# Kernel optimization log

Measured on AMD Instinct MI355X. Metric: run time of the kernel, lower is better.

Reference implementation:

```python
import jax, jax.numpy as jnp
import numpy as np

HIDDEN = 2048
N_HEADS = 32
N_KV_HEADS = 4
HEAD_DIM = 128
EPS = 1e-6
ROPE_THETA = 1000000.0
B, S = 1, 2048


def setup_inputs() -> dict:
    key = jax.random.key(0)
    ks = jax.random.split(key, 7)
    scale = 0.02
    return {
        "hidden_states": jax.random.normal(ks[0], (B, S, HIDDEN), jnp.float32),
        "wq": jax.random.normal(ks[1], (HIDDEN, N_HEADS * HEAD_DIM), jnp.float32) * scale,
        "wk": jax.random.normal(ks[2], (HIDDEN, N_KV_HEADS * HEAD_DIM), jnp.float32) * scale,
        "wv": jax.random.normal(ks[3], (HIDDEN, N_KV_HEADS * HEAD_DIM), jnp.float32) * scale,
        "wo": jax.random.normal(ks[4], (N_HEADS * HEAD_DIM, HIDDEN), jnp.float32) * scale,
        "q_norm_w": jnp.ones((HEAD_DIM,), jnp.float32),
        "k_norm_w": jnp.ones((HEAD_DIM,), jnp.float32),
    }


def _rmsnorm(x, w, eps=EPS):
    # RMSNorm over last (head_dim) axis, as in Qwen3MoeRMSNorm applied per-head
    var = jnp.mean(jnp.square(x), axis=-1, keepdims=True)
    return x * jax.lax.rsqrt(var + eps) * w


def _rope_cos_sin(seq_len, dtype):
    inv_freq = 1.0 / (ROPE_THETA ** (jnp.arange(0, HEAD_DIM, 2, dtype=jnp.float32) / HEAD_DIM))
    pos = jnp.arange(seq_len, dtype=jnp.float32)
    freqs = pos[:, None] * inv_freq[None, :]          # [S, dh/2]
    emb = jnp.concatenate([freqs, freqs], axis=-1)    # [S, dh]
    return jnp.cos(emb).astype(dtype), jnp.sin(emb).astype(dtype)


def _rotate_half(x):
    h = x.shape[-1] // 2
    return jnp.concatenate([-x[..., h:], x[..., :h]], axis=-1)


def reference(hidden_states, wq, wk, wv, wo, q_norm_w, k_norm_w):
    b, s, _ = hidden_states.shape
    # QKV projections (bias-free)
    q = (hidden_states @ wq).reshape(b, s, N_HEADS, HEAD_DIM)
    k = (hidden_states @ wk).reshape(b, s, N_KV_HEADS, HEAD_DIM)
    v = (hidden_states @ wv).reshape(b, s, N_KV_HEADS, HEAD_DIM)
    # per-head RMSNorm on Q and K
    q = _rmsnorm(q, q_norm_w)
    k = _rmsnorm(k, k_norm_w)
    # RoPE (prefill, start_pos = 0)
    cos, sin = _rope_cos_sin(s, q.dtype)              # [S, dh]
    cos = cos[None, :, None, :]
    sin = sin[None, :, None, :]
    q = q * cos + _rotate_half(q) * sin
    k = k * cos + _rotate_half(k) * sin
    # GQA: repeat KV heads to match Q heads
    groups = N_HEADS // N_KV_HEADS
    k = jnp.repeat(k, groups, axis=2)                 # [B,S,nH,dh]
    v = jnp.repeat(v, groups, axis=2)
    # causal SDPA
    scaling = HEAD_DIM ** -0.5
    scores = jnp.einsum("bqhd,bkhd->bhqk", q, k) * scaling
    causal = jnp.tril(jnp.ones((s, s), dtype=bool))
    scores = jnp.where(causal[None, None], scores, jnp.finfo(scores.dtype).min)
    probs = jax.nn.softmax(scores, axis=-1)
    attn = jnp.einsum("bhqk,bkhd->bqhd", probs, v)    # [B,S,nH,dh]
    attn = attn.reshape(b, s, N_HEADS * HEAD_DIM)
    return attn @ wo
```

## Files before the change

kernel.cpp:

```cpp
#include <hip/hip_runtime.h>
#include <stdint.h>

typedef unsigned short u16;
typedef __bf16 bf16x8 __attribute__((ext_vector_type(8)));
typedef float f32x4 __attribute__((ext_vector_type(4)));

#define SEQ 2048
#define QKV_N 5120
#define QN 4096

#if __has_builtin(__builtin_amdgcn_exp2f)
#define EXP2F __builtin_amdgcn_exp2f
#else
#define EXP2F exp2f
#endif

#define QSC (0.08838834764831845f * 1.4426950408889634f)
#define MLOG2E 17.312340490667560f

#define WAIT_VM(n) asm volatile("s_waitcnt vmcnt(" #n ")" ::: "memory")
#define WAIT_LGKM asm volatile("s_waitcnt lgkmcnt(0)" ::: "memory")
#define FENCE asm volatile("" ::: "memory")
#define BARRIER_RAW do { FENCE; __builtin_amdgcn_s_barrier(); FENCE; } while (0)

__device__ __forceinline__ u16 f2bf(float f) {
  union { float f; unsigned u; } v; v.f = f;
  unsigned r = v.u + 0x7fffu + ((v.u >> 16) & 1u);
  return (u16)(r >> 16);
}
__device__ __forceinline__ u16 f2bf_fast(float f) {
  union { float f; unsigned u; } v; v.f = f;
  return (u16)((v.u + 0x8000u) >> 16);
}
__device__ __forceinline__ float bf2f(u16 b) {
  union { unsigned u; float f; } v; v.u = ((unsigned)b) << 16;
  return v.f;
}

__device__ __forceinline__ void gl2lds16(const void* g, void* l) {
  __builtin_amdgcn_global_load_lds((const __attribute__((address_space(1))) void*)g,
                                   (__attribute__((address_space(3))) void*)l, 16, 0, 0);
}

__global__ __launch_bounds__(256) void k_prep(const float* __restrict__ hidden,
                                              const float* __restrict__ wq, const float* __restrict__ wk,
                                              const float* __restrict__ wv, const float* __restrict__ wo,
                                              u16* __restrict__ hid_bf, u16* __restrict__ WT,
                                              u16* __restrict__ woT) {
  __shared__ float t[32][33];
  int bx = blockIdx.x;
  if (bx < 4096) {
    int i = (bx * 256 + threadIdx.x) * 4;
    float4 v = *(const float4*)(hidden + i);
    ushort4 o;
    o.x = f2bf(v.x); o.y = f2bf(v.y); o.z = f2bf(v.z); o.w = f2bf(v.w);
    *(ushort4*)(hid_bf + i) = o;
    return;
  }
  const float* src; u16* dst; int R, C, cx, cy;
  if (bx < 4096 + 8192) {
    int local = bx - 4096; src = wq; dst = WT; R = 2048; C = 4096;
    cx = local & 127; cy = local >> 7;
  } else if (bx < 4096 + 8192 + 1024) {
    int local = bx - (4096 + 8192); src = wk; dst = WT + (size_t)4096 * 2048; R = 2048; C = 512;
    cx = local & 15; cy = local >> 4;
  } else if (bx < 4096 + 8192 + 2048) {
    int local = bx - (4096 + 8192 + 1024); src = wv; dst = WT + (size_t)4608 * 2048; R = 2048; C = 512;
    cx = local & 15; cy = local >> 4;
  } else {
    int local = bx - (4096 + 8192 + 2048); src = wo; dst = woT; R = 4096; C = 2048;
    cx = local & 63; cy = local >> 6;
  }
  int c0 = cx * 32, r0 = cy * 32;
  int j = threadIdx.x & 31, i0 = threadIdx.x >> 5;
#pragma unroll
  for (int p = 0; p < 4; ++p) {
    int r = i0 + p * 8;
    t[r][j] = src[(size_t)(r0 + r) * C + c0 + j];
  }
  __syncthreads();
#pragma unroll
  for (int p = 0; p < 4; ++p) {
    int r = i0 + p * 8;
    dst[(size_t)(c0 + r) * R + r0 + j] = f2bf(t[j][r]);
  }
}

__global__ __launch_bounds__(256) void k_gemm160(const u16* __restrict__ A, const u16* __restrict__ BT,
                                                 u16* __restrict__ C, int M, int N, int K) {
  __shared__ u16 As[2][128 * 64];
  __shared__ u16 Bs[2][160 * 64];
  const int tid = threadIdx.x;
  const int w = tid >> 6, lane = tid & 63, quad = lane >> 4, l15 = lane & 15;
  const int m0 = blockIdx.y * 128, n0 = blockIdx.x * 160;
  const int mw = (w & 1) * 64, nw = (w >> 1) * 80;

  f32x4 acc[4][5];
#pragma unroll
  for (int i = 0; i < 4; ++i)
#pragma unroll
    for (int j = 0; j < 5; ++j) acc[i][j] = {0.f, 0.f, 0.f, 0.f};

  auto stage = [&](int kt, int buf) {
    const int k0 = kt << 6;
#pragma unroll
    for (int p = 0; p < 4; ++p) {
      int ci = (w * 4 + p) * 64 + lane;
      int row = ci >> 3, gc = (ci & 7) ^ (row & 7);
      gl2lds16(A + (size_t)(m0 + row) * K + k0 + gc * 8, &As[buf][(w * 4 + p) * 512]);
    }
#pragma unroll
    for (int p = 0; p < 5; ++p) {
      int ci = (w * 5 + p) * 64 + lane;
      int row = ci >> 3, gc = (ci & 7) ^ (row & 7);
      gl2lds16(BT + (size_t)(n0 + row) * K + k0 + gc * 8, &Bs[buf][(w * 5 + p) * 512]);
    }
  };

  const int nk = K >> 6;
  stage(0, 0);
  for (int kt = 0; kt < nk; ++kt) {
    WAIT_LGKM;
    BARRIER_RAW;
    if (kt + 1 < nk) {
      stage(kt + 1, (kt + 1) & 1);
      WAIT_VM(9);
    } else {
      WAIT_VM(0);
    }
    BARRIER_RAW;
    const u16* Ac = As[kt & 1];
    const u16* Bc = Bs[kt & 1];
#pragma unroll
    for (int kk = 0; kk < 2; ++kk) {
      bf16x8 a[4], b[5];
#pragma unroll
      for (int mt = 0; mt < 4; ++mt) {
        int row = mw + mt * 16 + l15;
        a[mt] = *(const bf16x8*)(Ac + row * 64 + (((kk * 4 + quad) ^ (row & 7)) * 8));
      }
#pragma unroll
      for (int nt = 0; nt < 5; ++nt) {
        int row = nw + nt * 16 + l15;
        b[nt] = *(const bf16x8*)(Bc + row * 64 + (((kk * 4 + quad) ^ (row & 7)) * 8));
      }
#pragma unroll
      for (int mt = 0; mt < 4; ++mt)
#pragma unroll
        for (int nt = 0; nt < 5; ++nt)
          acc[mt][nt] = __builtin_amdgcn_mfma_f32_16x16x32_bf16(a[mt], b[nt], acc[mt][nt], 0, 0, 0);
    }
  }
#pragma unroll
  for (int mt = 0; mt < 4; ++mt)
#pragma unroll
    for (int nt = 0; nt < 5; ++nt)
#pragma unroll
      for (int r = 0; r < 4; ++r) {
        int row = m0 + mw + mt * 16 + quad * 4 + r;
        int col = n0 + nw + nt * 16 + l15;
        C[(size_t)row * N + col] = f2bf(acc[mt][nt][r]);
      }
}

__global__ __launch_bounds__(256) void k_gemm_sk(const u16* __restrict__ A, const u16* __restrict__ BT,
                                                 float* __restrict__ C, int M, int N, int K) {
  __shared__ u16 As[2][128 * 64];
  __shared__ u16 Bs[2][128 * 64];
  const int tid = threadIdx.x;
  const int w = tid >> 6, lane = tid & 63, quad = lane >> 4, l15 = lane & 15;
  const int m0 = blockIdx.y * 128, n0 = blockIdx.x * 128;
  const int mw = (w & 1) * 64, nw = (w >> 1) * 64;
  const int khalf = K >> 1;
  const int kbase = blockIdx.z * khalf;

  f32x4 acc[4][4];
#pragma unroll
  for (int i = 0; i < 4; ++i)
#pragma unroll
    for (int j = 0; j < 4; ++j) acc[i][j] = {0.f, 0.f, 0.f, 0.f};

  auto stage = [&](int kt, int buf) {
    const int k0 = kbase + (kt << 6);
#pragma unroll
    for (int p = 0; p < 4; ++p) {
      int ci = (w * 4 + p) * 64 + lane;
      int row = ci >> 3, gc = (ci & 7) ^ (row & 7);
      gl2lds16(A + (size_t)(m0 + row) * K + k0 + gc * 8, &As[buf][(w * 4 + p) * 512]);
      gl2lds16(BT + (size_t)(n0 + row) * K + k0 + gc * 8, &Bs[buf][(w * 4 + p) * 512]);
    }
  };

  const int nk = khalf >> 6;
  stage(0, 0);
  for (int kt = 0; kt < nk; ++kt) {
    WAIT_LGKM;
    BARRIER_RAW;
    if (kt + 1 < nk) {
      stage(kt + 1, (kt + 1) & 1);
      WAIT_VM(8);
    } else {
      WAIT_VM(0);
    }
    BARRIER_RAW;
    const u16* Ac = As[kt & 1];
    const u16* Bc = Bs[kt & 1];
#pragma unroll
    for (int kk = 0; kk < 2; ++kk) {
      bf16x8 a[4], b[4];
#pragma unroll
      for (int mt = 0; mt < 4; ++mt) {
        int row = mw + mt * 16 + l15;
        a[mt] = *(const bf16x8*)(Ac + row * 64 + (((kk * 4 + quad) ^ (row & 7)) * 8));
      }
#pragma unroll
      for (int nt = 0; nt < 4; ++nt) {
        int row = nw + nt * 16 + l15;
        b[nt] = *(const bf16x8*)(Bc + row * 64 + (((kk * 4 + quad) ^ (row & 7)) * 8));
      }
#pragma unroll
      for (int mt = 0; mt < 4; ++mt)
#pragma unroll
        for (int nt = 0; nt < 4; ++nt)
          acc[mt][nt] = __builtin_amdgcn_mfma_f32_16x16x32_bf16(a[mt], b[nt], acc[mt][nt], 0, 0, 0);
    }
  }
#pragma unroll
  for (int mt = 0; mt < 4; ++mt)
#pragma unroll
    for (int nt = 0; nt < 4; ++nt)
#pragma unroll
      for (int r = 0; r < 4; ++r) {
        int row = m0 + mw + mt * 16 + quad * 4 + r;
        int col = n0 + nw + nt * 16 + l15;
        atomicAdd(&C[(size_t)row * N + col], acc[mt][nt][r]);
      }
}

__global__ __launch_bounds__(256) void k_post(const u16* __restrict__ QKV,
                                              const float* __restrict__ qw, const float* __restrict__ kw,
                                              u16* __restrict__ qb, u16* __restrict__ kb,
                                              u16* __restrict__ vt) {
  __shared__ u16 t[32][34];
  int bx = blockIdx.x;
  if (bx < 2048) {
    int s = bx;
    int w = threadIdx.x >> 6, lane = threadIdx.x & 63;
    const u16* row = QKV + (size_t)s * QKV_N;
    float inv_freq = EXP2F(-(float)lane * (19.931568569324174f / 64.0f));
    float fr = (float)s * inv_freq;
    float sn, cs;
    __sincosf(fr, &sn, &cs);
    float qw0 = qw[lane], qw1 = qw[lane + 64];
    float kw0 = kw[lane], kw1 = kw[lane + 64];
    for (int item = w; item < 36; item += 4) {
      bool isq = item < 32;
      int h = isq ? item : item - 32;
      int base = isq ? h * 128 : 4096 + h * 128;
      float x0 = bf2f(row[base + lane]), x1 = bf2f(row[base + 64 + lane]);
      float ss = x0 * x0 + x1 * x1;
#pragma unroll
      for (int off = 1; off < 64; off <<= 1) ss += __shfl_xor(ss, off);
      float rr = rsqrtf(ss * (1.0f / 128.0f) + 1e-6f);
      float n0 = x0 * rr * (isq ? qw0 : kw0), n1 = x1 * rr * (isq ? qw1 : kw1);
      float y0 = n0 * cs - n1 * sn;
      float y1 = n1 * cs + n0 * sn;
      if (isq) {
        size_t o = (size_t)s * QN + h * 128 + lane;
        qb[o] = f2bf(y0 * QSC);
        qb[o + 64] = f2bf(y1 * QSC);
      } else {
        size_t o = ((size_t)h * SEQ + s) * 128 + lane;
        kb[o] = f2bf(y0);
        kb[o + 64] = f2bf(y1);
      }
    }
    return;
  }
  int local = bx - 2048;
  int s0 = (local & 63) * 32, d0 = ((local >> 6) & 3) * 32, h = local >> 8;
  int j = threadIdx.x & 31, i0 = threadIdx.x >> 5;
#pragma unroll
  for (int p = 0; p < 4; ++p) {
    int r = i0 + p * 8;
    t[r][j] = QKV[(size_t)(s0 + r) * QKV_N + 4608 + h * 128 + d0 + j];
  }
  __syncthreads();
#pragma unroll
  for (int p = 0; p < 4; ++p) {
    int r = i0 + p * 8;
    vt[((size_t)h * 128 + d0 + r) * SEQ + s0 + j] = t[j][r];
  }
}

__global__ __launch_bounds__(256, 2) void k_flash(const u16* __restrict__ qb_, const u16* __restrict__ kb,
                                                  const u16* __restrict__ vt, u16* __restrict__ attn) {
  __shared__ u16 Ks[2][64 * 128];
  __shared__ u16 Vts[2][128 * 64];
  __shared__ u16 Ps[4][2048];
  const int bx = blockIdx.x;
  const int head = bx & 31;
  const int a = bx >> 5;
  const int kvh = head >> 3;
  const int tid = threadIdx.x, w = tid >> 6, lane = tid & 63, quad = lane >> 4, l15 = lane & 15;
  const int rA = a * 64 + w * 16;
  const int rB = (31 - a) * 64 + w * 16;

  bf16x8 qf[2][4];
#pragma unroll
  for (int mt = 0; mt < 2; ++mt) {
    const int rbase = mt ? rB : rA;
    const u16* qrow = qb_ + (size_t)(rbase + l15) * QN + head * 128;
#pragma unroll
    for (int ks = 0; ks < 4; ++ks) qf[mt][ks] = *(const bf16x8*)(qrow + ks * 32 + quad * 8);
  }
  f32x4 o[2][8];
#pragma unroll
  for (int mt = 0; mt < 2; ++mt)
#pragma unroll
    for (int i = 0; i < 8; ++i) o[mt][i] = {0.f, 0.f, 0.f, 0.f};
  float lr[2][4] = {{0.f, 0.f, 0.f, 0.f}, {0.f, 0.f, 0.f, 0.f}};

  const u16* kbase = kb + (size_t)kvh * SEQ * 128;
  const u16* vbase = vt + (size_t)kvh * 128 * SEQ;
  u16* pw = Ps[w];

  auto stage = [&](int ti, int buf) {
    const int t0 = ti * 64;
#pragma unroll
    for (int p = 0; p < 4; ++p) {
      int ci = (w * 4 + p) * 64 + lane;
      {
        int row = ci >> 4, gc = (ci & 15) ^ (row & 15);
        gl2lds16(kbase + (size_t)(t0 + row) * 128 + gc * 8, &Ks[buf][(w * 4 + p) * 512]);
      }
      {
        int d = ci >> 3, gc = (ci & 7) ^ (d & 7);
        gl2lds16(vbase + (size_t)d * SEQ + t0 + gc * 8, &Vts[buf][(w * 4 + p) * 512]);
      }
    }
  };

  const int nT = 32 - a;
  stage(0, 0);
  for (int ti = 0; ti < nT; ++ti) {
    const int t0 = ti * 64;
    WAIT_LGKM;
    BARRIER_RAW;
    if (ti + 1 < nT) {
      stage(ti + 1, (ti + 1) & 1);
      WAIT_VM(8);
    } else {
      WAIT_VM(0);
    }
    BARRIER_RAW;
    const u16* Kc = Ks[ti & 1];
    const u16* Vc = Vts[ti & 1];

    const bool aA = t0 < rA + 16;
    {
      f32x4 sa[2][4];
#pragma unroll
      for (int mt = 0; mt < 2; ++mt)
#pragma unroll
        for (int nt = 0; nt < 4; ++nt) sa[mt][nt] = {0.f, 0.f, 0.f, 0.f};
#pragma unroll
      for (int nt = 0; nt < 4; ++nt) {
        int row = nt * 16 + l15;
#pragma unroll
        for (int ks = 0; ks < 4; ++ks) {
          bf16x8 kf = *(const bf16x8*)(Kc + row * 128 + (((ks * 4 + quad) ^ (row & 15)) * 8));
          if (aA) sa[0][nt] = __builtin_amdgcn_mfma_f32_16x16x32_bf16(qf[0][ks], kf, sa[0][nt], 0, 0, 0);
          sa[1][nt] = __builtin_amdgcn_mfma_f32_16x16x32_bf16(qf[1][ks], kf, sa[1][nt], 0, 0, 0);
        }
      }
#pragma unroll
      for (int mt = 0; mt < 2; ++mt) {
        if (mt == 0 && !aA) continue;
        const int rl = mt ? rB : rA;
        const bool domask = (t0 + 63 > rl);
        u16* pm = pw + mt * 1024;
#pragma unroll
        for (int nt = 0; nt < 4; ++nt)
#pragma unroll
          for (int r = 0; r < 4; ++r) {
            float p = EXP2F(sa[mt][nt][r] - MLOG2E);
            if (domask) {
              int tcol = t0 + nt * 16 + l15;
              int qrow = rl + quad * 4 + r;
              p = (tcol > qrow) ? 0.f : p;
            }
            sa[mt][nt][r] = p;
            pm[(quad * 4 + r) * 64 + ((nt ^ quad) << 4) + l15] = f2bf_fast(p);
          }
#pragma unroll
        for (int r = 0; r < 4; ++r)
          lr[mt][r] += sa[mt][0][r] + sa[mt][1][r] + sa[mt][2][r] + sa[mt][3][r];
      }
      WAIT_LGKM;
#pragma unroll
      for (int ks2 = 0; ks2 < 2; ++ks2) {
        int col = (ks2 * 32 + quad * 8) ^ ((l15 >> 2) << 4);
        bf16x8 pa0, pa1;
        if (aA) pa0 = *(const bf16x8*)(pw + l15 * 64 + col);
        pa1 = *(const bf16x8*)(pw + 1024 + l15 * 64 + col);
#pragma unroll
        for (int nt2 = 0; nt2 < 8; ++nt2) {
          int d = nt2 * 16 + l15;
          bf16x8 vf = *(const bf16x8*)(Vc + d * 64 + (((ks2 * 4 + quad) ^ (d & 7)) * 8));
          if (aA) o[0][nt2] = __builtin_amdgcn_mfma_f32_16x16x32_bf16(pa0, vf, o[0][nt2], 0, 0, 0);
          o[1][nt2] = __builtin_amdgcn_mfma_f32_16x16x32_bf16(pa1, vf, o[1][nt2], 0, 0, 0);
        }
      }
    }
  }
#pragma unroll
  for (int mt = 0; mt < 2; ++mt) {
    const int rbase = mt ? rB : rA;
    float inv[4];
#pragma unroll
    for (int r = 0; r < 4; ++r) {
      float s = lr[mt][r];
      s += __shfl_xor(s, 1);
      s += __shfl_xor(s, 2);
      s += __shfl_xor(s, 4);
      s += __shfl_xor(s, 8);
      inv[r] = 1.0f / s;
    }
#pragma unroll
    for (int nt2 = 0; nt2 < 8; ++nt2)
#pragma unroll
      for (int r = 0; r < 4; ++r) {
        size_t idx = (size_t)(rbase + quad * 4 + r) * QN + head * 128 + nt2 * 16 + l15;
        attn[idx] = f2bf_fast(o[mt][nt2][r] * inv[r]);
      }
  }
}

extern "C" void kernel_launch(void* const* d_in, const int* in_sizes, int n_in,
                              void* d_out, int out_size, void* d_ws, size_t ws_size,
                              hipStream_t stream) {
  const float* hidden = (const float*)d_in[0];
  const float* wq = (const float*)d_in[1];
  const float* wk = (const float*)d_in[2];
  const float* wv = (const float*)d_in[3];
  const float* wo = (const float*)d_in[4];
  const float* qnw = (const float*)d_in[5];
  const float* knw = (const float*)d_in[6];
  float* out = (float*)d_out;

  char* ws = (char*)d_ws;
  u16* hid_bf = (u16*)(ws);
  u16* WT = (u16*)(ws + 8388608);
  u16* woT = (u16*)(ws + 29360128);
  u16* QKV = (u16*)(ws + 46137344);
  u16* q_bf = (u16*)(ws + 88080384);
  u16* k_bf = (u16*)(ws + 104857600);
  u16* vt = (u16*)(ws + 106954752);
  u16* attn = (u16*)(ws + 109051904);

  hipMemsetAsync(d_out, 0, (size_t)2048 * 2048 * 4, stream);
  k_prep<<<22528, 256, 0, stream>>>(hidden, wq, wk, wv, wo, hid_bf, WT, woT);
  k_gemm160<<<dim3(32, 16), 256, 0, stream>>>(hid_bf, WT, QKV, 2048, 5120, 2048);
  k_post<<<3072, 256, 0, stream>>>(QKV, qnw, knw, q_bf, k_bf, vt);
  k_flash<<<512, 256, 0, stream>>>(q_bf, k_bf, vt, attn);
  k_gemm_sk<<<dim3(16, 16, 2), 256, 0, stream>>>(attn, woT, out, 2048, 2048, 4096);
}
```

Baseline: 323.8 us.

## Restructure flash attention to 128-row Q tiles with 8 waves and 128-key tiles

The flash kernel moves from 4-wave blocks that each handle a paired light and heavy 64-row Q tile to 8-wave blocks that each handle one 128-row Q tile. Blocks are ordered heaviest first, and K/V tiles grow to 128 keys. K stays double-buffered, while V becomes single-buffered and is loaded during the QK^T and softmax phase. s_setprio is raised around the MFMA loops. This is meant to double K/V reuse in LDS per block and cut per-tile overhead, at the cost of losing the causal pairing balance and of more LDS per block (about 104KB), which limits occupancy.

Measured after the change: 304.2 us. 6.0% less time.

```diff
diff --git a/kernel.cpp b/kernel.cpp
--- a/kernel.cpp
+++ b/kernel.cpp
@@ -293,148 +293,136 @@
   }
 }
 
-__global__ __launch_bounds__(256, 2) void k_flash(const u16* __restrict__ qb_, const u16* __restrict__ kb,
-                                                  const u16* __restrict__ vt, u16* __restrict__ attn) {
-  __shared__ u16 Ks[2][64 * 128];
-  __shared__ u16 Vts[2][128 * 64];
-  __shared__ u16 Ps[4][2048];
+__global__ __launch_bounds__(512) void k_flash(const u16* __restrict__ qb_, const u16* __restrict__ kb,
+                                               const u16* __restrict__ vt, u16* __restrict__ attn) {
+  __shared__ u16 Ks[2][128 * 128];
+  __shared__ u16 Vts[128 * 128];
+  __shared__ u16 Ps[8][16 * 128];
   const int bx = blockIdx.x;
   const int head = bx & 31;
-  const int a = bx >> 5;
+  const int qblk = 15 - (bx >> 5);
   const int kvh = head >> 3;
+  const int q0 = qblk * 128;
   const int tid = threadIdx.x, w = tid >> 6, lane = tid & 63, quad = lane >> 4, l15 = lane & 15;
-  const int rA = a * 64 + w * 16;
-  const int rB = (31 - a) * 64 + w * 16;
-
-  bf16x8 qf[2][4];
-#pragma unroll
-  for (int mt = 0; mt < 2; ++mt) {
-    const int rbase = mt ? rB : rA;
-    const u16* qrow = qb_ + (size_t)(rbase + l15) * QN + head * 128;
-#pragma unroll
-    for (int ks = 0; ks < 4; ++ks) qf[mt][ks] = *(const bf16x8*)(qrow + ks * 32 + quad * 8);
-  }
-  f32x4 o[2][8];
-#pragma unroll
-  for (int mt = 0; mt < 2; ++mt)
-#pragma unroll
-    for (int i = 0; i < 8; ++i) o[mt][i] = {0.f, 0.f, 0.f, 0.f};
-  float lr[2][4] = {{0.f, 0.f, 0.f, 0.f}, {0.f, 0.f, 0.f, 0.f}};
+  const int qrow0 = q0 + w * 16;
+
+  bf16x8 qf[4];
+  {
+    const u16* qrow = qb_ + (size_t)(qrow0 + l15) * QN + head * 128;
+#pragma unroll
+    for (int ks = 0; ks < 4; ++ks) qf[ks] = *(const bf16x8*)(qrow + ks * 32 + quad * 8);
+  }
+  f32x4 o[8];
+#pragma unroll
+  for (int i = 0; i < 8; ++i) o[i] = {0.f, 0.f, 0.f, 0.f};
+  float lr[4] = {0.f, 0.f, 0.f, 0.f};
 
   const u16* kbase = kb + (size_t)kvh * SEQ * 128;
   const u16* vbase = vt + (size_t)kvh * 128 * SEQ;
   u16* pw = Ps[w];
 
-  auto stage = [&](int ti, int buf) {
-    const int t0 = ti * 64;
+  auto stageK = [&](int ti, int buf) {
+    const int t0 = ti * 128;
 #pragma unroll
     for (int p = 0; p < 4; ++p) {
       int ci = (w * 4 + p) * 64 + lane;
-      {
-        int row = ci >> 4, gc = (ci & 15) ^ (row & 15);
-        gl2lds16(kbase + (size_t)(t0 + row) * 128 + gc * 8, &Ks[buf][(w * 4 + p) * 512]);
-      }
-      {
-        int d = ci >> 3, gc = (ci & 7) ^ (d & 7);
-        gl2lds16(vbase + (size_t)d * SEQ + t0 + gc * 8, &Vts[buf][(w * 4 + p) * 512]);
-      }
+      int row = ci >> 4, gc = (ci & 15) ^ (row & 15);
+      gl2lds16(kbase + (size_t)(t0 + row) * 128 + gc * 8, &Ks[buf][(w * 4 + p) * 512]);
     }
   };
-
-  const int nT = 32 - a;
-  stage(0, 0);
+  auto stageV = [&](int ti) {
+    const int t0 = ti * 128;
+#pragma unroll
+    for (int p = 0; p < 4; ++p) {
+      int ci = (w * 4 + p) * 64 + lane;
+      int d = ci >> 4, gc = (ci & 15) ^ (d & 15);
+      gl2lds16(vbase + (size_t)d * SEQ + t0 + gc * 8, &Vts[(w * 4 + p) * 512]);
+    }
+  };
+
+  const int nT = qblk + 1;
+  stageK(0, 0);
   for (int ti = 0; ti < nT; ++ti) {
-    const int t0 = ti * 64;
+    const int t0 = ti * 128;
+    const bool more = (ti + 1 < nT);
     WAIT_LGKM;
     BARRIER_RAW;
-    if (ti + 1 < nT) {
-      stage(ti + 1, (ti + 1) & 1);
-      WAIT_VM(8);
-    } else {
-      WAIT_VM(0);
-    }
+    if (more) stageK(ti + 1, (ti + 1) & 1);
+    stageV(ti);
+    if (more) { WAIT_VM(8); } else { WAIT_VM(4); }
     BARRIER_RAW;
     const u16* Kc = Ks[ti & 1];
-    const u16* Vc = Vts[ti & 1];
-
-    const bool aA = t0 < rA + 16;
-    {
-      f32x4 sa[2][4];
-#pragma unroll
-      for (int mt = 0; mt < 2; ++mt)
-#pragma unroll
-        for (int nt = 0; nt < 4; ++nt) sa[mt][nt] = {0.f, 0.f, 0.f, 0.f};
-#pragma unroll
-      for (int nt = 0; nt < 4; ++nt) {
-        int row = nt * 16 + l15;
-#pragma unroll
-        for (int ks = 0; ks < 4; ++ks) {
-          bf16x8 kf = *(const bf16x8*)(Kc + row * 128 + (((ks * 4 + quad) ^ (row & 15)) * 8));
-          if (aA) sa[0][nt] = __builtin_amdgcn_mfma_f32_16x16x32_bf16(qf[0][ks], kf, sa[0][nt], 0, 0, 0);
-          sa[1][nt] = __builtin_amdgcn_mfma_f32_16x16x32_bf16(qf[1][ks], kf, sa[1][nt], 0, 0, 0);
+
+    f32x4 sa[8];
+#pragma unroll
+    for (int nt = 0; nt < 8; ++nt) sa[nt] = {0.f, 0.f, 0.f, 0.f};
+    __builtin_amdgcn_s_setprio(1);
+#pragma unroll
+    for (int nt = 0; nt < 8; ++nt) {
+      int row = nt * 16 + l15;
+#pragma unroll
+      for (int ks = 0; ks < 4; ++ks) {
+        bf16x8 kf = *(const bf16x8*)(Kc + row * 128 + (((ks * 4 + quad) ^ (row & 15)) * 8));
+        sa[nt] = __builtin_amdgcn_mfma_f32_16x16x32_bf16(qf[ks], kf, sa[nt], 0, 0, 0);
+      }
+    }
+    __builtin_amdgcn_s_setprio(0);
+
+    const bool domask = (ti == nT - 1);
+#pragma unroll
+    for (int nt = 0; nt < 8; ++nt)
+#pragma unroll
+      for (int r = 0; r < 4; ++r) {
+        float p = EXP2F(sa[nt][r] - MLOG2E);
+        if (domask) {
+          int tcol = t0 + nt * 16 + l15;
+          int qr = qrow0 + quad * 4 + r;
+          p = (tcol > qr) ? 0.f : p;
         }
-      }
-#pragma unroll
-      for (int mt = 0; mt < 2; ++mt) {
-        if (mt == 0 && !aA) continue;
-        const int rl = mt ? rB : rA;
-        const bool domask = (t0 + 63 > rl);
-        u16* pm = pw + mt * 1024;
-#pragma unroll
-        for (int nt = 0; nt < 4; ++nt)
-#pragma unroll
-          for (int r = 0; r < 4; ++r) {
-            float p = EXP2F(sa[mt][nt][r] - MLOG2E);
-            if (domask) {
-              int tcol = t0 + nt * 16 + l15;
-              int qrow = rl + quad * 4 + r;
-              p = (tcol > qrow) ? 0.f : p;
-            }
-            sa[mt][nt][r] = p;
-            pm[(quad * 4 + r) * 64 + ((nt ^ quad) << 4) + l15] = f2bf_fast(p);
-          }
-#pragma unroll
-        for (int r = 0; r < 4; ++r)
-          lr[mt][r] += sa[mt][0][r] + sa[mt][1][r] + sa[mt][2][r] + sa[mt][3][r];
-      }
-      WAIT_LGKM;
-#pragma unroll
-      for (int ks2 = 0; ks2 < 2; ++ks2) {
-        int col = (ks2 * 32 + quad * 8) ^ ((l15 >> 2) << 4);
-        bf16x8 pa0, pa1;
-        if (aA) pa0 = *(const bf16x8*)(pw + l15 * 64 + col);
-        pa1 = *(const bf16x8*)(pw + 1024 + l15 * 64 + col);
-#pragma unroll
-        for (int nt2 = 0; nt2 < 8; ++nt2) {
-          int d = nt2 * 16 + l15;
-          bf16x8 vf = *(const bf16x8*)(Vc + d * 64 + (((ks2 * 4 + quad) ^ (d & 7)) * 8));
-          if (aA) o[0][nt2] = __builtin_amdgcn_mfma_f32_16x16x32_bf16(pa0, vf, o[0][nt2], 0, 0, 0);
-          o[1][nt2] = __builtin_amdgcn_mfma_f32_16x16x32_bf16(pa1, vf, o[1][nt2], 0, 0, 0);
-        }
-      }
-    }
-  }
-#pragma unroll
-  for (int mt = 0; mt < 2; ++mt) {
-    const int rbase = mt ? rB : rA;
-    float inv[4];
+        sa[nt][r] = p;
+        pw[(quad * 4 + r) * 128 + ((nt ^ quad) << 4) + l15] = f2bf_fast(p);
+      }
+#pragma unroll
+    for (int r = 0; r < 4; ++r)
+      lr[r] += ((sa[0][r] + sa[1][r]) + (sa[2][r] + sa[3][r])) +
+               ((sa[4][r] + sa[5][r]) + (sa[6][r] + sa[7][r]));
+
+    if (more) { WAIT_VM(4); } else { WAIT_VM(0); }
+    BARRIER_RAW;
+    WAIT_LGKM;
+
+    __builtin_amdgcn_s_setprio(1);
+#pragma unroll
+    for (int ks2 = 0; ks2 < 4; ++ks2) {
+      int col = (ks2 * 32 + quad * 8) ^ ((l15 & 12) << 2);
+      bf16x8 pa = *(const bf16x8*)(pw + l15 * 128 + col);
+#pragma unroll
+      for (int nt2 = 0; nt2 < 8; ++nt2) {
+        int d = nt2 * 16 + l15;
+        bf16x8 vf = *(const bf16x8*)(Vts + d * 128 + (((ks2 * 4 + quad) ^ (d & 15)) * 8));
+        o[nt2] = __builtin_amdgcn_mfma_f32_16x16x32_bf16(pa, vf, o[nt2], 0, 0, 0);
+      }
+    }
+    __builtin_amdgcn_s_setprio(0);
+  }
+
+  float inv[4];
+#pragma unroll
+  for (int r = 0; r < 4; ++r) {
+    float s = lr[r];
+    s += __shfl_xor(s, 1);
+    s += __shfl_xor(s, 2);
+    s += __shfl_xor(s, 4);
+    s += __shfl_xor(s, 8);
+    inv[r] = 1.0f / s;
+  }
+#pragma unroll
+  for (int nt2 = 0; nt2 < 8; ++nt2)
 #pragma unroll
     for (int r = 0; r < 4; ++r) {
-      float s = lr[mt][r];
-      s += __shfl_xor(s, 1);
-      s += __shfl_xor(s, 2);
-      s += __shfl_xor(s, 4);
-      s += __shfl_xor(s, 8);
-      inv[r] = 1.0f / s;
-    }
-#pragma unroll
-    for (int nt2 = 0; nt2 < 8; ++nt2)
-#pragma unroll
-      for (int r = 0; r < 4; ++r) {
-        size_t idx = (size_t)(rbase + quad * 4 + r) * QN + head * 128 + nt2 * 16 + l15;
-        attn[idx] = f2bf_fast(o[mt][nt2][r] * inv[r]);
-      }
-  }
+      size_t idx = (size_t)(qrow0 + quad * 4 + r) * QN + head * 128 + nt2 * 16 + l15;
+      attn[idx] = f2bf_fast(o[nt2][r] * inv[r]);
+    }
 }
 
 extern "C" void kernel_launch(void* const* d_in, const int* in_sizes, int n_in,
@@ -463,6 +451,6 @@
   k_prep<<<22528, 256, 0, stream>>>(hidden, wq, wk, wv, wo, hid_bf, WT, woT);
   k_gemm160<<<dim3(32, 16), 256, 0, stream>>>(hid_bf, WT, QKV, 2048, 5120, 2048);
   k_post<<<3072, 256, 0, stream>>>(QKV, qnw, knw, q_bf, k_bf, vt);
-  k_flash<<<512, 256, 0, stream>>>(q_bf, k_bf, vt, attn);
+  k_flash<<<512, 512, 0, stream>>>(q_bf, k_bf, vt, attn);
   k_gemm_sk<<<dim3(16, 16, 2), 256, 0, stream>>>(attn, woT, out, 2048, 2048, 4096);
 }
```
